# Kernel tuning notes

Hardware: AMD Instinct MI355X
Metric: run time of the kernel (lower is better)

## Reference

```python
import jax, jax.numpy as jnp
import numpy as np


def _sq_dist(q, k):
    # pairwise squared L2 distance: [B,H,L,D] x [B,H,M,D] -> [B,H,L,M]
    q2 = jnp.sum(q * q, axis=-1)[..., :, None]
    k2 = jnp.sum(k * k, axis=-1)[..., None, :]
    qk = jnp.einsum('bhld,bhmd->bhlm', q, k)
    return q2 + k2 - 2.0 * qk


def setup_inputs() -> dict:
    key = jax.random.key(0)
    k1, k2, k3 = jax.random.split(key, 3)
    B, H, L, D = 2, 8, 2048, 64
    query = jax.random.normal(k1, (B, H, L, D), dtype=jnp.float32)
    key_t = jax.random.normal(k2, (B, H, L, D), dtype=jnp.float32)
    mask = jnp.ones((B, L), dtype=jnp.float32)
    # mu param: normal(0, 0.5) * [0,1][:,None,None] -> first component zeroed
    mu = (jax.random.normal(k3, (2, H, D), dtype=jnp.float32) * 0.5
          * jnp.array([0.0, 1.0], dtype=jnp.float32)[:, None, None])
    pi = jnp.array([0.5, 0.5], dtype=jnp.float32)
    return {'query': query, 'key': key_t, 'mask': mask, 'mu': mu, 'pi': pi}


def reference(query, key, mask, mu, pi):
    D = query.shape[-1]
    var = D ** 0.5  # self.var = head_dim ** 0.5
    neg = 1e6 * (1.0 - mask[:, None, None, :])  # [B,1,1,L]
    pic = jnp.clip(pi, 0.0, 1.0)
    qk1 = (-0.5 / var) * _sq_dist(query, key - mu[0][None, :, None, :]) - neg
    qk2 = (-0.5 / var) * _sq_dist(query, key - mu[1][None, :, None, :]) - neg
    attn = jnp.exp(qk1) * pic[0] + jnp.exp(qk2) * pic[1]
    return attn / jnp.sum(attn, axis=-1, keepdims=True)
```

## Files before the change

### kernel.cpp

```cpp
#include <hip/hip_runtime.h>
#include <math.h>

#define B_ 2
#define H_ 8
#define L_ 2048
#define D_ 64
#define BM 32
#define BN 128
#define NJ (L_ / BN)
#define NT 512
#define L2E 1.4426950408889634f

typedef _Float16 half8 __attribute__((ext_vector_type(8)));
typedef __attribute__((ext_vector_type(4))) float f4;

typedef __attribute__((address_space(3))) void lds_void_t;
typedef const __attribute__((address_space(1))) void gbl_void_t;
#define GLL16(gp, lp) __builtin_amdgcn_global_load_lds( \
    (gbl_void_t*)(gp), (lds_void_t*)(lp), 16, 0, 0)

#define MFMA16F(a, b, c) __builtin_amdgcn_mfma_f32_16x16x32_f16(a, b, c, 0, 0, 0)

struct LdsT {
  half8  kth[BN * 8];
  float2 cka[L_];
  float  muv[2][D_];
  float  er0[BM], er1[BM];
  float  red[4][BM];
};

__device__ inline half8 cvt8(const float4& a0, const float4& a1) {
  half8 r;
  r[0] = (_Float16)a0.x; r[1] = (_Float16)a0.y;
  r[2] = (_Float16)a0.z; r[3] = (_Float16)a0.w;
  r[4] = (_Float16)a1.x; r[5] = (_Float16)a1.y;
  r[6] = (_Float16)a1.z; r[7] = (_Float16)a1.w;
  return r;
}

__global__ __launch_bounds__(256) void prep_kernel(
    const float* __restrict__ k, const float* __restrict__ mask,
    const float* __restrict__ mu, float2* __restrict__ ck,
    half8* __restrict__ wh)
{
  int bh = blockIdx.x >> 3;
  int c  = (blockIdx.x & 7) * 256 + threadIdx.x;
  int b  = bh >> 3, h = bh & 7;
  const float s = -0.0625f;
  const float* kp  = k  + ((size_t)bh * L_ + c) * D_;
  const float* mu0 = mu + (size_t)h * D_;
  const float* mu1 = mu + (size_t)(H_ * D_) + (size_t)h * D_;
  float x[D_];
#pragma unroll
  for (int d = 0; d < D_; d += 4)
    *reinterpret_cast<float4*>(&x[d]) = *reinterpret_cast<const float4*>(kp + d);
  float s0 = 0.f, s1 = 0.f;
#pragma unroll
  for (int d = 0; d < D_; ++d) {
    float a = x[d] - mu0[d]; s0 += a * a;
    float bb = x[d] - mu1[d]; s1 += bb * bb;
  }
  float neg = 1.0e6f * (1.0f - mask[(size_t)b * L_ + c]);
  ck[(size_t)bh * L_ + c] = make_float2(exp2f((s * s0 - neg) * L2E),
                                        exp2f((s * s1 - neg) * L2E));
#pragma unroll
  for (int gp = 0; gp < 8; ++gp) {
    int g = gp ^ (c & 7);
    wh[((size_t)bh * L_ + c) * 8 + gp] =
        cvt8(*reinterpret_cast<const float4*>(&x[8 * g]),
             *reinterpret_cast<const float4*>(&x[8 * g + 4]));
  }
}

template <bool USE_WS>
__global__ __launch_bounds__(NT, 8) void mg_kernel(
    const float* __restrict__ q, const float* __restrict__ kk,
    const float* __restrict__ mask, const float* __restrict__ mu,
    const float* __restrict__ pi, const float2* __restrict__ ckw,
    const half8* __restrict__ wh, float* __restrict__ out)
{
  extern __shared__ __align__(16) char smem_raw[];
  LdsT& S = *reinterpret_cast<LdsT*>(smem_raw);
  const int t = threadIdx.x;
  int bid = blockIdx.x;
  int vwg = (bid & 7) * 128 + (bid >> 3);
  int bh  = vwg >> 6;
  int rb  = vwg & 63;
  int b = bh >> 3, h = bh & 7;
  int row0 = rb * BM;

  const int w  = t >> 6;
  const int ln = t & 63;
  const int ci = ln & 15;
  const int kg = ln >> 4;
  const int x7 = ci & 7;
  const int wc = w & 3;
  const int wr = (w >> 2) * 16;

  const float s   = -0.0625f;
  const float DDC = 0.125f * L2E;

  const float*  maskb = mask + (size_t)b * L_;
  const float2* ckb   = ckw + (size_t)bh * L_;
  const float4* kb4   = (const float4*)(kk + (size_t)bh * L_ * D_);
  const half8*  whb   = wh + (size_t)bh * (L_ * 8);

  if (t < 2 * D_)
    S.muv[t >> 6][t & 63] =
        mu[(size_t)(t >> 6) * (H_ * D_) + (size_t)h * D_ + (t & 63)];

  if (USE_WS) {
#pragma unroll
    for (int i = 0; i < 4; ++i) {
      int u = t + NT * i;
      S.cka[u] = ckb[u];
    }
  }

  half8 ah[2];
  {
    const float* qrow = q + ((size_t)bh * L_ + row0 + wr + ci) * D_;
#pragma unroll
    for (int h2 = 0; h2 < 2; ++h2) {
      float4 a0 = *reinterpret_cast<const float4*>(qrow + 32 * h2 + kg * 8);
      float4 a1 = *reinterpret_cast<const float4*>(qrow + 32 * h2 + kg * 8 + 4);
      ah[h2] = cvt8(a0, a1);
    }
  }
  __syncthreads();

  if (t < BM) {
    float pi0 = fminf(fmaxf(pi[0], 0.f), 1.f);
    float pi1 = fminf(fmaxf(pi[1], 0.f), 1.f);
    const float* qr = q + ((size_t)bh * L_ + row0 + t) * D_;
    float a0 = 0.f, a1 = 0.f, a2 = 0.f;
#pragma unroll
    for (int dq = 0; dq < 16; ++dq) {
      float4 qv = *reinterpret_cast<const float4*>(qr + 4 * dq);
      a0 += qv.x * qv.x + qv.y * qv.y + qv.z * qv.z + qv.w * qv.w;
      a1 += qv.x * S.muv[0][4*dq] + qv.y * S.muv[0][4*dq+1] +
            qv.z * S.muv[0][4*dq+2] + qv.w * S.muv[0][4*dq+3];
      a2 += qv.x * S.muv[1][4*dq] + qv.y * S.muv[1][4*dq+1] +
            qv.z * S.muv[1][4*dq+2] + qv.w * S.muv[1][4*dq+3];
    }
    S.er0[t] = pi0 * exp2f((s * a0 + 2.f * s * a1) * L2E);
    S.er1[t] = pi1 * exp2f((s * a0 + 2.f * s * a2) * L2E);
  }
  __syncthreads();

  float e0r[4], e1r[4];
#pragma unroll
  for (int reg = 0; reg < 4; ++reg) {
    e0r[reg] = S.er0[wr + kg * 4 + reg];
    e1r[reg] = S.er1[wr + kg * 4 + reg];
  }

  auto STAGE = [&](int j) {
    if (USE_WS) {
#pragma unroll
      for (int i = 0; i < 2; ++i)
        GLL16(whb + (size_t)j * (BN * 8) + t + NT * i, &S.kth[t + NT * i]);
    } else {
#pragma unroll
      for (int i = 0; i < 2; ++i) {
        int u = t + NT * i;
        int col = u >> 3, gp = u & 7, g = gp ^ (col & 7);
        float4 x0 = kb4[(size_t)(j * BN + col) * 16 + 2 * g];
        float4 x1 = kb4[(size_t)(j * BN + col) * 16 + 2 * g + 1];
        S.kth[u] = cvt8(x0, x1);
      }
      if (t < BN) {
        const float* kc = kk + ((size_t)bh * L_ + j * BN + t) * D_;
        float s0 = 0.f, s1 = 0.f;
#pragma unroll
        for (int dq = 0; dq < 16; ++dq) {
          float4 kv = *reinterpret_cast<const float4*>(kc + 4 * dq);
          float a;
          a = kv.x - S.muv[0][4*dq];   s0 += a * a;
          a = kv.y - S.muv[0][4*dq+1]; s0 += a * a;
          a = kv.z - S.muv[0][4*dq+2]; s0 += a * a;
          a = kv.w - S.muv[0][4*dq+3]; s0 += a * a;
          a = kv.x - S.muv[1][4*dq];   s1 += a * a;
          a = kv.y - S.muv[1][4*dq+1]; s1 += a * a;
          a = kv.z - S.muv[1][4*dq+2]; s1 += a * a;
          a = kv.w - S.muv[1][4*dq+3]; s1 += a * a;
        }
        float neg = 1.0e6f * (1.0f - maskb[j * BN + t]);
        S.cka[j * BN + t] = make_float2(exp2f((s * s0 - neg) * L2E),
                                        exp2f((s * s1 - neg) * L2E));
      }
    }
  };

  float rsum[4] = {0.f, 0.f, 0.f, 0.f};
#pragma unroll 1
  for (int j = 0; j < NJ; ++j) {
    __syncthreads();
    STAGE(j);
    __syncthreads();
    float2 ec[2];
#pragma unroll
    for (int n = 0; n < 2; ++n)
      ec[n] = S.cka[j * BN + wc * 32 + 16 * n + ci];
#pragma unroll
    for (int n = 0; n < 2; ++n) {
      int base = (wc * 32 + n * 16 + ci) * 8;
      half8 b0 = S.kth[base + (kg ^ x7)];
      half8 b1 = S.kth[base + ((4 + kg) ^ x7)];
      f4 acc = {0.f, 0.f, 0.f, 0.f};
      acc = MFMA16F(ah[0], b0, acc);
      acc = MFMA16F(ah[1], b1, acc);
#pragma unroll
      for (int reg = 0; reg < 4; ++reg) {
        float g2 = __builtin_amdgcn_exp2f(DDC * acc[reg]);
        float m  = fmaf(e0r[reg], ec[n].x, e1r[reg] * ec[n].y);
        rsum[reg] = fmaf(g2, m, rsum[reg]);
      }
    }
  }

#pragma unroll
  for (int reg = 0; reg < 4; ++reg) {
    float v = rsum[reg];
    v += __shfl_xor(v, 1, 64);
    v += __shfl_xor(v, 2, 64);
    v += __shfl_xor(v, 4, 64);
    v += __shfl_xor(v, 8, 64);
    if (ci == 0) S.red[wc][wr + kg * 4 + reg] = v;
  }
  __syncthreads();
#pragma unroll
  for (int reg = 0; reg < 4; ++reg) {
    int r = wr + kg * 4 + reg;
    float inv = 1.0f / (S.red[0][r] + S.red[1][r] + S.red[2][r] + S.red[3][r]);
    e0r[reg] *= inv;
    e1r[reg] *= inv;
  }

  float* ob = out + ((size_t)bh * L_ + row0 + wr + kg * 4) * L_ + wc * 32 + ci;
#pragma unroll 1
  for (int jj = 0; jj < NJ; ++jj) {
    const int j = NJ - 1 - jj;
    if (jj != 0) {
      __syncthreads();
      STAGE(j);
      __syncthreads();
    }
    float2 ec[2];
#pragma unroll
    for (int n = 0; n < 2; ++n)
      ec[n] = S.cka[j * BN + wc * 32 + 16 * n + ci];
#pragma unroll
    for (int n = 0; n < 2; ++n) {
      int base = (wc * 32 + n * 16 + ci) * 8;
      half8 b0 = S.kth[base + (kg ^ x7)];
      half8 b1 = S.kth[base + ((4 + kg) ^ x7)];
      f4 acc = {0.f, 0.f, 0.f, 0.f};
      acc = MFMA16F(ah[0], b0, acc);
      acc = MFMA16F(ah[1], b1, acc);
#pragma unroll
      for (int reg = 0; reg < 4; ++reg) {
        float g2 = __builtin_amdgcn_exp2f(DDC * acc[reg]);
        float m  = fmaf(e0r[reg], ec[n].x, e1r[reg] * ec[n].y);
        float p  = g2 * m;
        __builtin_nontemporal_store(
            p, ob + (size_t)reg * L_ + (j * BN + n * 16));
      }
    }
  }
}

extern "C" void kernel_launch(void* const* d_in, const int* in_sizes, int n_in,
                              void* d_out, int out_size, void* d_ws, size_t ws_size,
                              hipStream_t stream) {
  const float* q    = (const float*)d_in[0];
  const float* k    = (const float*)d_in[1];
  const float* mask = (const float*)d_in[2];
  const float* mu   = (const float*)d_in[3];
  const float* pi   = (const float*)d_in[4];
  float* out = (float*)d_out;

  const size_t smem     = sizeof(LdsT);
  const size_t ck_bytes = (size_t)B_ * H_ * L_ * sizeof(float2);
  const size_t wp_bytes = (size_t)B_ * H_ * L_ * D_ * sizeof(short);
  const bool use_ws = (ws_size >= ck_bytes + wp_bytes) && (d_ws != nullptr);

  if (use_ws) {
    float2* ck = (float2*)d_ws;
    half8*  wh = (half8*)((char*)d_ws + ck_bytes);
    (void)hipFuncSetAttribute(reinterpret_cast<const void*>(&mg_kernel<true>),
                              hipFuncAttributeMaxDynamicSharedMemorySize, (int)smem);
    prep_kernel<<<dim3(B_ * H_ * 8), dim3(256), 0, stream>>>(k, mask, mu, ck, wh);
    mg_kernel<true><<<dim3(B_ * H_ * (L_ / BM)), dim3(NT), smem, stream>>>(
        q, k, mask, mu, pi, ck, wh, out);
  } else {
    (void)hipFuncSetAttribute(reinterpret_cast<const void*>(&mg_kernel<false>),
                              hipFuncAttributeMaxDynamicSharedMemorySize, (int)smem);
    mg_kernel<false><<<dim3(B_ * H_ * (L_ / BM)), dim3(NT), smem, stream>>>(
        q, k, mask, mu, pi, nullptr, nullptr, out);
  }
}
```

Measured before the change: 114.0 us.

## Double-buffer K tiles via register prefetch and read ck terms from global

Replaces the synchronous global_load_lds staging of each K tile with a register-prefetched, double-buffered LDS scheme. The tile two steps ahead is loaded into registers while the next buffer is written, which removes one barrier per iteration and overlaps global loads with MFMA and exp work. The per-column ck factors are now read straight from global instead of being preloaded into a 16KB LDS array, shrinking the LDS footprint. The cost is more register pressure, one more LDS buffer, and scattered small global reads of ck inside the loop.

```diff
diff --git a/kernel.cpp b/kernel.cpp
--- a/kernel.cpp
+++ b/kernel.cpp
@@ -14,16 +14,11 @@
 typedef _Float16 half8 __attribute__((ext_vector_type(8)));
 typedef __attribute__((ext_vector_type(4))) float f4;
 
-typedef __attribute__((address_space(3))) void lds_void_t;
-typedef const __attribute__((address_space(1))) void gbl_void_t;
-#define GLL16(gp, lp) __builtin_amdgcn_global_load_lds( \
-    (gbl_void_t*)(gp), (lds_void_t*)(lp), 16, 0, 0)
-
 #define MFMA16F(a, b, c) __builtin_amdgcn_mfma_f32_16x16x32_f16(a, b, c, 0, 0, 0)
 
 struct LdsT {
-  half8  kth[BN * 8];
-  float2 cka[L_];
+  half8  kth[2][BN * 8];
+  float2 ckt[BN];
   float  muv[2][D_];
   float  er0[BM], er1[BM];
   float  red[4][BM];
@@ -103,19 +98,11 @@
   const float*  maskb = mask + (size_t)b * L_;
   const float2* ckb   = ckw + (size_t)bh * L_;
   const float4* kb4   = (const float4*)(kk + (size_t)bh * L_ * D_);
-  const half8*  whb   = wh + (size_t)bh * (L_ * 8);
+  const float4* whb4  = (const float4*)(wh + (size_t)bh * (L_ * 8));
 
   if (t < 2 * D_)
     S.muv[t >> 6][t & 63] =
         mu[(size_t)(t >> 6) * (H_ * D_) + (size_t)h * D_ + (t & 63)];
-
-  if (USE_WS) {
-#pragma unroll
-    for (int i = 0; i < 4; ++i) {
-      int u = t + NT * i;
-      S.cka[u] = ckb[u];
-    }
-  }
 
   half8 ah[2];
   {
@@ -127,6 +114,9 @@
       ah[h2] = cvt8(a0, a1);
     }
   }
+
+  float4 v0, v1;
+  if (USE_WS) { v0 = whb4[t]; v1 = whb4[t + NT]; }
   __syncthreads();
 
   if (t < BM) {
@@ -146,6 +136,13 @@
     S.er0[t] = pi0 * exp2f((s * a0 + 2.f * s * a1) * L2E);
     S.er1[t] = pi1 * exp2f((s * a0 + 2.f * s * a2) * L2E);
   }
+
+  if (USE_WS) {
+    S.kth[0][t]      = __builtin_bit_cast(half8, v0);
+    S.kth[0][t + NT] = __builtin_bit_cast(half8, v1);
+    v0 = whb4[(BN * 8) + t];
+    v1 = whb4[(BN * 8) + t + NT];
+  }
   __syncthreads();
 
   float e0r[4], e1r[4];
@@ -155,58 +152,67 @@
     e1r[reg] = S.er1[wr + kg * 4 + reg];
   }
 
-  auto STAGE = [&](int j) {
-    if (USE_WS) {
-#pragma unroll
-      for (int i = 0; i < 2; ++i)
-        GLL16(whb + (size_t)j * (BN * 8) + t + NT * i, &S.kth[t + NT * i]);
-    } else {
-#pragma unroll
-      for (int i = 0; i < 2; ++i) {
-        int u = t + NT * i;
-        int col = u >> 3, gp = u & 7, g = gp ^ (col & 7);
-        float4 x0 = kb4[(size_t)(j * BN + col) * 16 + 2 * g];
-        float4 x1 = kb4[(size_t)(j * BN + col) * 16 + 2 * g + 1];
-        S.kth[u] = cvt8(x0, x1);
-      }
-      if (t < BN) {
-        const float* kc = kk + ((size_t)bh * L_ + j * BN + t) * D_;
-        float s0 = 0.f, s1 = 0.f;
-#pragma unroll
-        for (int dq = 0; dq < 16; ++dq) {
-          float4 kv = *reinterpret_cast<const float4*>(kc + 4 * dq);
-          float a;
-          a = kv.x - S.muv[0][4*dq];   s0 += a * a;
-          a = kv.y - S.muv[0][4*dq+1]; s0 += a * a;
-          a = kv.z - S.muv[0][4*dq+2]; s0 += a * a;
-          a = kv.w - S.muv[0][4*dq+3]; s0 += a * a;
-          a = kv.x - S.muv[1][4*dq];   s1 += a * a;
-          a = kv.y - S.muv[1][4*dq+1]; s1 += a * a;
-          a = kv.z - S.muv[1][4*dq+2]; s1 += a * a;
-          a = kv.w - S.muv[1][4*dq+3]; s1 += a * a;
-        }
-        float neg = 1.0e6f * (1.0f - maskb[j * BN + t]);
-        S.cka[j * BN + t] = make_float2(exp2f((s * s0 - neg) * L2E),
-                                        exp2f((s * s1 - neg) * L2E));
-      }
+  auto STAGE_FB = [&](int j) {
+#pragma unroll
+    for (int i = 0; i < 2; ++i) {
+      int u = t + NT * i;
+      int col = u >> 3, gp = u & 7, g = gp ^ (col & 7);
+      float4 x0 = kb4[(size_t)(j * BN + col) * 16 + 2 * g];
+      float4 x1 = kb4[(size_t)(j * BN + col) * 16 + 2 * g + 1];
+      S.kth[0][u] = cvt8(x0, x1);
+    }
+    if (t < BN) {
+      const float* kc = kk + ((size_t)bh * L_ + j * BN + t) * D_;
+      float s0 = 0.f, s1 = 0.f;
+#pragma unroll
+      for (int dq = 0; dq < 16; ++dq) {
+        float4 kv = *reinterpret_cast<const float4*>(kc + 4 * dq);
+        float a;
+        a = kv.x - S.muv[0][4*dq];   s0 += a * a;
+        a = kv.y - S.muv[0][4*dq+1]; s0 += a * a;
+        a = kv.z - S.muv[0][4*dq+2]; s0 += a * a;
+        a = kv.w - S.muv[0][4*dq+3]; s0 += a * a;
+        a = kv.x - S.muv[1][4*dq];   s1 += a * a;
+        a = kv.y - S.muv[1][4*dq+1]; s1 += a * a;
+        a = kv.z - S.muv[1][4*dq+2]; s1 += a * a;
+        a = kv.w - S.muv[1][4*dq+3]; s1 += a * a;
+      }
+      float neg = 1.0e6f * (1.0f - maskb[j * BN + t]);
+      S.ckt[t] = make_float2(exp2f((s * s0 - neg) * L2E),
+                             exp2f((s * s1 - neg) * L2E));
     }
   };
 
   float rsum[4] = {0.f, 0.f, 0.f, 0.f};
+  int cur = 0;
 #pragma unroll 1
   for (int j = 0; j < NJ; ++j) {
-    __syncthreads();
-    STAGE(j);
-    __syncthreads();
     float2 ec[2];
-#pragma unroll
-    for (int n = 0; n < 2; ++n)
-      ec[n] = S.cka[j * BN + wc * 32 + 16 * n + ci];
+    if (USE_WS) {
+      if (j + 1 < NJ) {
+        S.kth[cur ^ 1][t]      = __builtin_bit_cast(half8, v0);
+        S.kth[cur ^ 1][t + NT] = __builtin_bit_cast(half8, v1);
+      }
+      if (j + 2 < NJ) {
+        v0 = whb4[(size_t)(j + 2) * (BN * 8) + t];
+        v1 = whb4[(size_t)(j + 2) * (BN * 8) + t + NT];
+      }
+#pragma unroll
+      for (int n = 0; n < 2; ++n)
+        ec[n] = ckb[j * BN + wc * 32 + 16 * n + ci];
+    } else {
+      __syncthreads();
+      STAGE_FB(j);
+      __syncthreads();
+#pragma unroll
+      for (int n = 0; n < 2; ++n) ec[n] = S.ckt[wc * 32 + 16 * n + ci];
+    }
+    const int rbuf = USE_WS ? cur : 0;
 #pragma unroll
     for (int n = 0; n < 2; ++n) {
       int base = (wc * 32 + n * 16 + ci) * 8;
-      half8 b0 = S.kth[base + (kg ^ x7)];
-      half8 b1 = S.kth[base + ((4 + kg) ^ x7)];
+      half8 b0 = S.kth[rbuf][base + (kg ^ x7)];
+      half8 b1 = S.kth[rbuf][base + ((4 + kg) ^ x7)];
       f4 acc = {0.f, 0.f, 0.f, 0.f};
       acc = MFMA16F(ah[0], b0, acc);
       acc = MFMA16F(ah[1], b1, acc);
@@ -217,6 +223,12 @@
         rsum[reg] = fmaf(g2, m, rsum[reg]);
       }
     }
+    if (USE_WS) { __syncthreads(); cur ^= 1; }
+  }
+
+  if (USE_WS && NJ >= 3) {
+    v0 = whb4[(size_t)(NJ - 3) * (BN * 8) + t];
+    v1 = whb4[(size_t)(NJ - 3) * (BN * 8) + t + NT];
   }
 
 #pragma unroll
@@ -238,23 +250,38 @@
   }
 
   float* ob = out + ((size_t)bh * L_ + row0 + wr + kg * 4) * L_ + wc * 32 + ci;
+  cur = 1;
 #pragma unroll 1
   for (int jj = 0; jj < NJ; ++jj) {
     const int j = NJ - 1 - jj;
-    if (jj != 0) {
-      __syncthreads();
-      STAGE(j);
-      __syncthreads();
-    }
     float2 ec[2];
-#pragma unroll
-    for (int n = 0; n < 2; ++n)
-      ec[n] = S.cka[j * BN + wc * 32 + 16 * n + ci];
+    if (USE_WS) {
+      if (jj >= 1 && j >= 1) {
+        S.kth[cur ^ 1][t]      = __builtin_bit_cast(half8, v0);
+        S.kth[cur ^ 1][t + NT] = __builtin_bit_cast(half8, v1);
+      }
+      if (j >= 2) {
+        v0 = whb4[(size_t)(j - 2) * (BN * 8) + t];
+        v1 = whb4[(size_t)(j - 2) * (BN * 8) + t + NT];
+      }
+#pragma unroll
+      for (int n = 0; n < 2; ++n)
+        ec[n] = ckb[j * BN + wc * 32 + 16 * n + ci];
+    } else {
+      if (jj != 0) {
+        __syncthreads();
+        STAGE_FB(j);
+        __syncthreads();
+      }
+#pragma unroll
+      for (int n = 0; n < 2; ++n) ec[n] = S.ckt[wc * 32 + 16 * n + ci];
+    }
+    const int rbuf = USE_WS ? cur : 0;
 #pragma unroll
     for (int n = 0; n < 2; ++n) {
       int base = (wc * 32 + n * 16 + ci) * 8;
-      half8 b0 = S.kth[base + (kg ^ x7)];
-      half8 b1 = S.kth[base + ((4 + kg) ^ x7)];
+      half8 b0 = S.kth[rbuf][base + (kg ^ x7)];
+      half8 b1 = S.kth[rbuf][base + ((4 + kg) ^ x7)];
       f4 acc = {0.f, 0.f, 0.f, 0.f};
       acc = MFMA16F(ah[0], b0, acc);
       acc = MFMA16F(ah[1], b1, acc);
@@ -267,6 +294,7 @@
             p, ob + (size_t)reg * L_ + (j * BN + n * 16));
       }
     }
+    if (USE_WS) { __syncthreads(); cur ^= 1; }
   }
 }
 
```

Measured after the change: 124.8 us. +9.5%, slower.

## Drop LDS staging of keys; load key fragments directly from global per wave

Applied to the files above, without the earlier changes.

Removes the shared-memory staging of fp16 key tiles and per-column constants, along with the barriers around each stage. Each wave now owns a 512-column slice and reads its MFMA B fragments and column constants straight from global memory (L2). The row tile shrinks to 16 with 256 threads, doubling the grid, and the prep kernel drops the XOR swizzle. This removes sync and LDS traffic but relies on L2 bandwidth for repeated key reads and loses explicit reuse across waves.

```diff
diff --git a/kernel.cpp b/kernel.cpp
--- a/kernel.cpp
+++ b/kernel.cpp
@@ -5,28 +5,20 @@
 #define H_ 8
 #define L_ 2048
 #define D_ 64
-#define BM 32
-#define BN 128
-#define NJ (L_ / BN)
-#define NT 512
+#define BM 16
+#define NT 256
+#define NBLK 32
 #define L2E 1.4426950408889634f
 
 typedef _Float16 half8 __attribute__((ext_vector_type(8)));
 typedef __attribute__((ext_vector_type(4))) float f4;
 
-typedef __attribute__((address_space(3))) void lds_void_t;
-typedef const __attribute__((address_space(1))) void gbl_void_t;
-#define GLL16(gp, lp) __builtin_amdgcn_global_load_lds( \
-    (gbl_void_t*)(gp), (lds_void_t*)(lp), 16, 0, 0)
-
 #define MFMA16F(a, b, c) __builtin_amdgcn_mfma_f32_16x16x32_f16(a, b, c, 0, 0, 0)
 
 struct LdsT {
-  half8  kth[BN * 8];
-  float2 cka[L_];
-  float  muv[2][D_];
-  float  er0[BM], er1[BM];
-  float  red[4][BM];
+  float muv[2][D_];
+  float er0[BM], er1[BM];
+  float red[4][BM];
 };
 
 __device__ inline half8 cvt8(const float4& a0, const float4& a1) {
@@ -64,12 +56,10 @@
   ck[(size_t)bh * L_ + c] = make_float2(exp2f((s * s0 - neg) * L2E),
                                         exp2f((s * s1 - neg) * L2E));
 #pragma unroll
-  for (int gp = 0; gp < 8; ++gp) {
-    int g = gp ^ (c & 7);
-    wh[((size_t)bh * L_ + c) * 8 + gp] =
+  for (int g = 0; g < 8; ++g)
+    wh[((size_t)bh * L_ + c) * 8 + g] =
         cvt8(*reinterpret_cast<const float4*>(&x[8 * g]),
              *reinterpret_cast<const float4*>(&x[8 * g + 4]));
-  }
 }
 
 template <bool USE_WS>
@@ -79,13 +69,12 @@
     const float* __restrict__ pi, const float2* __restrict__ ckw,
     const half8* __restrict__ wh, float* __restrict__ out)
 {
-  extern __shared__ __align__(16) char smem_raw[];
-  LdsT& S = *reinterpret_cast<LdsT*>(smem_raw);
+  __shared__ LdsT S;
   const int t = threadIdx.x;
   int bid = blockIdx.x;
-  int vwg = (bid & 7) * 128 + (bid >> 3);
-  int bh  = vwg >> 6;
-  int rb  = vwg & 63;
+  int vwg = (bid & 7) * 256 + (bid >> 3);
+  int bh  = vwg >> 7;
+  int rb  = vwg & 127;
   int b = bh >> 3, h = bh & 7;
   int row0 = rb * BM;
 
@@ -93,33 +82,21 @@
   const int ln = t & 63;
   const int ci = ln & 15;
   const int kg = ln >> 4;
-  const int x7 = ci & 7;
-  const int wc = w & 3;
-  const int wr = (w >> 2) * 16;
 
   const float s   = -0.0625f;
   const float DDC = 0.125f * L2E;
 
   const float*  maskb = mask + (size_t)b * L_;
   const float2* ckb   = ckw + (size_t)bh * L_;
-  const float4* kb4   = (const float4*)(kk + (size_t)bh * L_ * D_);
   const half8*  whb   = wh + (size_t)bh * (L_ * 8);
 
   if (t < 2 * D_)
     S.muv[t >> 6][t & 63] =
         mu[(size_t)(t >> 6) * (H_ * D_) + (size_t)h * D_ + (t & 63)];
 
-  if (USE_WS) {
-#pragma unroll
-    for (int i = 0; i < 4; ++i) {
-      int u = t + NT * i;
-      S.cka[u] = ckb[u];
-    }
-  }
-
   half8 ah[2];
   {
-    const float* qrow = q + ((size_t)bh * L_ + row0 + wr + ci) * D_;
+    const float* qrow = q + ((size_t)bh * L_ + row0 + ci) * D_;
 #pragma unroll
     for (int h2 = 0; h2 < 2; ++h2) {
       float4 a0 = *reinterpret_cast<const float4*>(qrow + 32 * h2 + kg * 8);
@@ -151,71 +128,58 @@
   float e0r[4], e1r[4];
 #pragma unroll
   for (int reg = 0; reg < 4; ++reg) {
-    e0r[reg] = S.er0[wr + kg * 4 + reg];
-    e1r[reg] = S.er1[wr + kg * 4 + reg];
-  }
-
-  auto STAGE = [&](int j) {
+    e0r[reg] = S.er0[kg * 4 + reg];
+    e1r[reg] = S.er1[kg * 4 + reg];
+  }
+
+  auto LOADCOL = [&](int col, half8& b0, half8& b1, float2& ec) {
     if (USE_WS) {
-#pragma unroll
-      for (int i = 0; i < 2; ++i)
-        GLL16(whb + (size_t)j * (BN * 8) + t + NT * i, &S.kth[t + NT * i]);
+      ec = ckb[col];
+      b0 = whb[(size_t)col * 8 + kg];
+      b1 = whb[(size_t)col * 8 + 4 + kg];
     } else {
-#pragma unroll
-      for (int i = 0; i < 2; ++i) {
-        int u = t + NT * i;
-        int col = u >> 3, gp = u & 7, g = gp ^ (col & 7);
-        float4 x0 = kb4[(size_t)(j * BN + col) * 16 + 2 * g];
-        float4 x1 = kb4[(size_t)(j * BN + col) * 16 + 2 * g + 1];
-        S.kth[u] = cvt8(x0, x1);
+      const float* kp = kk + ((size_t)bh * L_ + col) * D_;
+      float4 x0 = *reinterpret_cast<const float4*>(kp + 8 * kg);
+      float4 x1 = *reinterpret_cast<const float4*>(kp + 8 * kg + 4);
+      float4 x2 = *reinterpret_cast<const float4*>(kp + 32 + 8 * kg);
+      float4 x3 = *reinterpret_cast<const float4*>(kp + 32 + 8 * kg + 4);
+      b0 = cvt8(x0, x1);
+      b1 = cvt8(x2, x3);
+      int d0 = 8 * kg, d1 = 32 + 8 * kg;
+      float s0 = 0.f, s1 = 0.f;
+      float xs[8] = {x0.x, x0.y, x0.z, x0.w, x1.x, x1.y, x1.z, x1.w};
+      float ys[8] = {x2.x, x2.y, x2.z, x2.w, x3.x, x3.y, x3.z, x3.w};
+#pragma unroll
+      for (int i = 0; i < 8; ++i) {
+        float a;
+        a = xs[i] - S.muv[0][d0 + i]; s0 += a * a;
+        a = xs[i] - S.muv[1][d0 + i]; s1 += a * a;
+        a = ys[i] - S.muv[0][d1 + i]; s0 += a * a;
+        a = ys[i] - S.muv[1][d1 + i]; s1 += a * a;
       }
-      if (t < BN) {
-        const float* kc = kk + ((size_t)bh * L_ + j * BN + t) * D_;
-        float s0 = 0.f, s1 = 0.f;
-#pragma unroll
-        for (int dq = 0; dq < 16; ++dq) {
-          float4 kv = *reinterpret_cast<const float4*>(kc + 4 * dq);
-          float a;
-          a = kv.x - S.muv[0][4*dq];   s0 += a * a;
-          a = kv.y - S.muv[0][4*dq+1]; s0 += a * a;
-          a = kv.z - S.muv[0][4*dq+2]; s0 += a * a;
-          a = kv.w - S.muv[0][4*dq+3]; s0 += a * a;
-          a = kv.x - S.muv[1][4*dq];   s1 += a * a;
-          a = kv.y - S.muv[1][4*dq+1]; s1 += a * a;
-          a = kv.z - S.muv[1][4*dq+2]; s1 += a * a;
-          a = kv.w - S.muv[1][4*dq+3]; s1 += a * a;
-        }
-        float neg = 1.0e6f * (1.0f - maskb[j * BN + t]);
-        S.cka[j * BN + t] = make_float2(exp2f((s * s0 - neg) * L2E),
-                                        exp2f((s * s1 - neg) * L2E));
-      }
+      s0 += __shfl_xor(s0, 16, 64); s0 += __shfl_xor(s0, 32, 64);
+      s1 += __shfl_xor(s1, 16, 64); s1 += __shfl_xor(s1, 32, 64);
+      float neg = 1.0e6f * (1.0f - maskb[col]);
+      ec = make_float2(exp2f((s * s0 - neg) * L2E),
+                       exp2f((s * s1 - neg) * L2E));
     }
   };
 
   float rsum[4] = {0.f, 0.f, 0.f, 0.f};
-#pragma unroll 1
-  for (int j = 0; j < NJ; ++j) {
-    __syncthreads();
-    STAGE(j);
-    __syncthreads();
-    float2 ec[2];
-#pragma unroll
-    for (int n = 0; n < 2; ++n)
-      ec[n] = S.cka[j * BN + wc * 32 + 16 * n + ci];
-#pragma unroll
-    for (int n = 0; n < 2; ++n) {
-      int base = (wc * 32 + n * 16 + ci) * 8;
-      half8 b0 = S.kth[base + (kg ^ x7)];
-      half8 b1 = S.kth[base + ((4 + kg) ^ x7)];
-      f4 acc = {0.f, 0.f, 0.f, 0.f};
-      acc = MFMA16F(ah[0], b0, acc);
-      acc = MFMA16F(ah[1], b1, acc);
-#pragma unroll
-      for (int reg = 0; reg < 4; ++reg) {
-        float g2 = __builtin_amdgcn_exp2f(DDC * acc[reg]);
-        float m  = fmaf(e0r[reg], ec[n].x, e1r[reg] * ec[n].y);
-        rsum[reg] = fmaf(g2, m, rsum[reg]);
-      }
+  const int colw = w * 512;
+#pragma unroll 2
+  for (int j = 0; j < NBLK; ++j) {
+    int col = colw + j * 16 + ci;
+    half8 b0, b1; float2 ec;
+    LOADCOL(col, b0, b1, ec);
+    f4 acc = {0.f, 0.f, 0.f, 0.f};
+    acc = MFMA16F(ah[0], b0, acc);
+    acc = MFMA16F(ah[1], b1, acc);
+#pragma unroll
+    for (int reg = 0; reg < 4; ++reg) {
+      float g2 = __builtin_amdgcn_exp2f(DDC * acc[reg]);
+      float m  = fmaf(e0r[reg], ec.x, e1r[reg] * ec.y);
+      rsum[reg] = fmaf(g2, m, rsum[reg]);
     }
   }
 
@@ -226,46 +190,32 @@
     v += __shfl_xor(v, 2, 64);
     v += __shfl_xor(v, 4, 64);
     v += __shfl_xor(v, 8, 64);
-    if (ci == 0) S.red[wc][wr + kg * 4 + reg] = v;
+    if (ci == 0) S.red[w][kg * 4 + reg] = v;
   }
   __syncthreads();
 #pragma unroll
   for (int reg = 0; reg < 4; ++reg) {
-    int r = wr + kg * 4 + reg;
+    int r = kg * 4 + reg;
     float inv = 1.0f / (S.red[0][r] + S.red[1][r] + S.red[2][r] + S.red[3][r]);
     e0r[reg] *= inv;
     e1r[reg] *= inv;
   }
 
-  float* ob = out + ((size_t)bh * L_ + row0 + wr + kg * 4) * L_ + wc * 32 + ci;
-#pragma unroll 1
-  for (int jj = 0; jj < NJ; ++jj) {
-    const int j = NJ - 1 - jj;
-    if (jj != 0) {
-      __syncthreads();
-      STAGE(j);
-      __syncthreads();
-    }
-    float2 ec[2];
-#pragma unroll
-    for (int n = 0; n < 2; ++n)
-      ec[n] = S.cka[j * BN + wc * 32 + 16 * n + ci];
-#pragma unroll
-    for (int n = 0; n < 2; ++n) {
-      int base = (wc * 32 + n * 16 + ci) * 8;
-      half8 b0 = S.kth[base + (kg ^ x7)];
-      half8 b1 = S.kth[base + ((4 + kg) ^ x7)];
-      f4 acc = {0.f, 0.f, 0.f, 0.f};
-      acc = MFMA16F(ah[0], b0, acc);
-      acc = MFMA16F(ah[1], b1, acc);
-#pragma unroll
-      for (int reg = 0; reg < 4; ++reg) {
-        float g2 = __builtin_amdgcn_exp2f(DDC * acc[reg]);
-        float m  = fmaf(e0r[reg], ec[n].x, e1r[reg] * ec[n].y);
-        float p  = g2 * m;
-        __builtin_nontemporal_store(
-            p, ob + (size_t)reg * L_ + (j * BN + n * 16));
-      }
+  float* ob = out + ((size_t)bh * L_ + row0 + kg * 4) * L_ + colw + ci;
+#pragma unroll 2
+  for (int j = 0; j < NBLK; ++j) {
+    int col = colw + j * 16 + ci;
+    half8 b0, b1; float2 ec;
+    LOADCOL(col, b0, b1, ec);
+    f4 acc = {0.f, 0.f, 0.f, 0.f};
+    acc = MFMA16F(ah[0], b0, acc);
+    acc = MFMA16F(ah[1], b1, acc);
+#pragma unroll
+    for (int reg = 0; reg < 4; ++reg) {
+      float g2 = __builtin_amdgcn_exp2f(DDC * acc[reg]);
+      float m  = fmaf(e0r[reg], ec.x, e1r[reg] * ec.y);
+      float p  = g2 * m;
+      __builtin_nontemporal_store(p, ob + (size_t)reg * L_ + j * 16);
     }
   }
 }
@@ -280,7 +230,6 @@
   const float* pi   = (const float*)d_in[4];
   float* out = (float*)d_out;
 
-  const size_t smem     = sizeof(LdsT);
   const size_t ck_bytes = (size_t)B_ * H_ * L_ * sizeof(float2);
   const size_t wp_bytes = (size_t)B_ * H_ * L_ * D_ * sizeof(short);
   const bool use_ws = (ws_size >= ck_bytes + wp_bytes) && (d_ws != nullptr);
@@ -288,15 +237,11 @@
   if (use_ws) {
     float2* ck = (float2*)d_ws;
     half8*  wh = (half8*)((char*)d_ws + ck_bytes);
-    (void)hipFuncSetAttribute(reinterpret_cast<const void*>(&mg_kernel<true>),
-                              hipFuncAttributeMaxDynamicSharedMemorySize, (int)smem);
     prep_kernel<<<dim3(B_ * H_ * 8), dim3(256), 0, stream>>>(k, mask, mu, ck, wh);
-    mg_kernel<true><<<dim3(B_ * H_ * (L_ / BM)), dim3(NT), smem, stream>>>(
+    mg_kernel<true><<<dim3(B_ * H_ * (L_ / BM)), dim3(NT), 0, stream>>>(
         q, k, mask, mu, pi, ck, wh, out);
   } else {
-    (void)hipFuncSetAttribute(reinterpret_cast<const void*>(&mg_kernel<false>),
-                              hipFuncAttributeMaxDynamicSharedMemorySize, (int)smem);
-    mg_kernel<false><<<dim3(B_ * H_ * (L_ / BM)), dim3(NT), smem, stream>>>(
+    mg_kernel<false><<<dim3(B_ * H_ * (L_ / BM)), dim3(NT), 0, stream>>>(
         q, k, mask, mu, pi, nullptr, nullptr, out);
   }
 }
```

After: 155.6 us. 1.37x slower.
